# Optimization experiments

Hardware: AMD Instinct MI355X
Metric: run time of the kernel (lower is better)

The kernel has to match this reference:

```python
import jax, jax.numpy as jnp
import numpy as np

H = 32
W = 32
N = H * W            # num_patches = 1024
DIM = 512
HEADS = 8
DH = 64              # dim_head
INNER = HEADS * DH
B = 4
GATE = -2.0          # fixed, requires_grad=False in the torch module
NEG_THRESH = 0.9


def _rel_pos_index_dis():
    # mirrors relative_pos_index_dis(height=32, weight=32)
    coords = np.stack(np.meshgrid(np.arange(H), np.arange(W), indexing='ij'))  # [2,H,W]
    flat = coords.reshape(2, -1)                      # [2, N]
    rel = flat[:, :, None] - flat[:, None, :]         # [2, N, N]
    rel = rel.transpose(1, 2, 0).copy()               # [N, N, 2]
    dis = (rel[..., 0].astype(np.float32) / H) ** 2 + (rel[..., 1].astype(np.float32) / W) ** 2
    rel[..., 0] += H - 1
    rel[..., 1] += W - 1
    rel[..., 0] *= 2 * W - 1
    idx = rel.sum(-1)
    return idx.astype(np.int32), dis.astype(np.float32)


def setup_inputs() -> dict:
    key = jax.random.key(0)
    ks = jax.random.split(key, 6)
    rpi, dis = _rel_pos_index_dis()
    return {
        'x': jax.random.normal(ks[0], (B, N, DIM), dtype=jnp.float32),
        'prob': jax.random.uniform(ks[1], (B, N), dtype=jnp.float32),
        'w_qkv': jax.random.normal(ks[2], (DIM, 3 * INNER), dtype=jnp.float32) * 0.02,
        'rpb_table': jax.random.normal(ks[3], ((2 * H - 1) * (2 * W - 1), HEADS), dtype=jnp.float32) * 0.02,
        'headsita': jnp.arange(1, HEADS + 1, dtype=jnp.float32) * 0.1,
        'w_thresh': jax.random.normal(ks[4], (DH,), dtype=jnp.float32) * 0.02,
        'w_out': jax.random.normal(ks[5], (INNER, DIM), dtype=jnp.float32) * 0.02,
        'b_out': jnp.zeros((DIM,), dtype=jnp.float32),
        'rpi': jnp.asarray(rpi),
        'dis': jnp.asarray(dis),
    }


def reference(x, prob, w_qkv, rpb_table, headsita, w_thresh, w_out, b_out, rpi, dis):
    b, n, _ = x.shape
    h = headsita.shape[0]
    d = w_thresh.shape[0]
    scale = d ** -0.5

    qkv = x @ w_qkv                                            # [b, n, 3*h*d]
    q, k, v = jnp.split(qkv, 3, axis=-1)
    to_heads = lambda t: t.reshape(b, n, h, d).transpose(0, 2, 1, 3)  # [b, h, n, d]
    q, k, v = to_heads(q), to_heads(k), to_heads(v)

    dots0 = jnp.einsum('bhid,bhjd->bhij', q, k) * scale        # [b, h, n, n]

    # RPE: table lookup bias + learned Gaussian distance bias
    rpb = rpb_table[rpi.reshape(-1)].reshape(n, n, h).transpose(2, 0, 1)  # [h, n, n]
    factor = 1.0 / (2.0 * headsita ** 2 + 1e-6)                # [h]
    pos = jnp.exp(-factor[:, None, None] * dis[None, :, :])    # [h, n, n]
    dots = dots0 + rpb[None] + 0.01 * pos[None]

    attn = jax.nn.softmax(dots, axis=-1)                       # [b, h, n, n]
    attn_max = attn.max(axis=-1)                               # [b, h, n]
    attn_min = attn.min(axis=-1)

    # per-query learned threshold, gated by sigmoid(gate)
    t = jax.nn.sigmoid(jnp.einsum('bhnd,d->bhn', q, w_thresh)) * jax.nn.sigmoid(GATE)
    thresh = attn_min + t * (attn_max - attn_min)               # [b, h, n]

    record = (attn - thresh[..., None] > 0).astype(attn.dtype)  # hard 0/1 mask
    # rows (queries) whose prob >= neg_thresh are fully zeroed (as in the torch code)
    record = record * (prob < NEG_THRESH)[:, None, :, None].astype(attn.dtype)

    deno = jnp.sum(attn * record, axis=-1)                      # [b, h, n]
    attn_p = attn * record / (deno[..., None] + 1e-6)

    out = jnp.einsum('bhij,bhjd->bhid', attn_p, v)              # [b, h, n, d]
    out = out.transpose(0, 2, 1, 3).reshape(b, n, h * d)
    out = out @ w_out + b_out                                   # [b, n, dim]
    return out, jax.nn.softmax(dots0, axis=-1)
```

## Files before the change

### kernel.cpp

```cpp
#include <hip/hip_runtime.h>


__device__ __forceinline__ float wsum(float v) {
#pragma unroll
  for (int off = 32; off > 0; off >>= 1) v += __shfl_xor(v, off, 64);
  return v;
}
__device__ __forceinline__ float wmaxr(float v) {
#pragma unroll
  for (int off = 32; off > 0; off >>= 1) v = fmaxf(v, __shfl_xor(v, off, 64));
  return v;
}
__device__ __forceinline__ float wminr(float v) {
#pragma unroll
  for (int off = 32; off > 0; off >>= 1) v = fminf(v, __shfl_xor(v, off, 64));
  return v;
}

__global__ __launch_bounds__(256) void gemm_f32_128(
    const float* __restrict__ A, const float* __restrict__ Bm,
    float* __restrict__ C, int M, int N, int K) {
  __shared__ float As[16][132];
  __shared__ float Bs[16][132];
  const int t = threadIdx.x;
  const int bm = blockIdx.y * 128;
  const int bn = blockIdx.x * 128;
  const int tx = t & 15;
  const int ty = t >> 4;

  float acc[8][8];
#pragma unroll
  for (int i = 0; i < 8; ++i)
#pragma unroll
    for (int j = 0; j < 8; ++j) acc[i][j] = 0.0f;

  const int mr = t >> 1;
  const int kc = (t & 1) * 8;
  const int kr = t >> 4;
  const int nc = (t & 15) * 8;

  for (int k0 = 0; k0 < K; k0 += 16) {
    const float4* asrc = (const float4*)&A[(size_t)(bm + mr) * K + k0 + kc];
    const float4 a0 = asrc[0], a1 = asrc[1];
    const float4* bsrc = (const float4*)&Bm[(size_t)(k0 + kr) * N + bn + nc];
    const float4 b0 = bsrc[0], b1 = bsrc[1];
    __syncthreads();
    As[kc + 0][mr] = a0.x; As[kc + 1][mr] = a0.y;
    As[kc + 2][mr] = a0.z; As[kc + 3][mr] = a0.w;
    As[kc + 4][mr] = a1.x; As[kc + 5][mr] = a1.y;
    As[kc + 6][mr] = a1.z; As[kc + 7][mr] = a1.w;
    *(float4*)&Bs[kr][nc] = b0;
    *(float4*)&Bs[kr][nc + 4] = b1;
    __syncthreads();
#pragma unroll
    for (int kk = 0; kk < 16; ++kk) {
      const float4 aLo = *(const float4*)&As[kk][ty * 4];
      const float4 aHi = *(const float4*)&As[kk][64 + ty * 4];
      const float4 bLo = *(const float4*)&Bs[kk][tx * 4];
      const float4 bHi = *(const float4*)&Bs[kk][64 + tx * 4];
      const float av[8] = {aLo.x, aLo.y, aLo.z, aLo.w, aHi.x, aHi.y, aHi.z, aHi.w};
      const float bv[8] = {bLo.x, bLo.y, bLo.z, bLo.w, bHi.x, bHi.y, bHi.z, bHi.w};
#pragma unroll
      for (int i = 0; i < 8; ++i)
#pragma unroll
        for (int j = 0; j < 8; ++j) acc[i][j] += av[i] * bv[j];
    }
  }

#pragma unroll
  for (int i = 0; i < 8; ++i) {
    const int row = bm + ((i < 4) ? (ty * 4 + i) : (64 + ty * 4 + (i - 4)));
    float4 lo, hi;
    lo.x = acc[i][0]; lo.y = acc[i][1]; lo.z = acc[i][2]; lo.w = acc[i][3];
    hi.x = acc[i][4]; hi.y = acc[i][5]; hi.z = acc[i][6]; hi.w = acc[i][7];
    *(float4*)&C[(size_t)row * N + bn + tx * 4] = lo;
    *(float4*)&C[(size_t)row * N + bn + 64 + tx * 4] = hi;
  }
}

__global__ __launch_bounds__(256, 2) void attn_fused(
    const float* __restrict__ qkv,
    const float* __restrict__ prob,
    const float* __restrict__ rpb,
    const float* __restrict__ headsita,
    const float* __restrict__ w_thresh,
    float* __restrict__ out2,
    float* __restrict__ attnout)
{
  __shared__ float kv_lds[128 * 64];
  __shared__ float q_t[64 * 32];
  __shared__ float multi[4096];

  const int t = threadIdx.x;
  const int w = t >> 6;
  const int l = t & 63;
  const int itile = blockIdx.x;
  const int bh = blockIdx.y;
  const int b = bh >> 3;
  const int h = bh & 7;
  const int i0 = itile * 32;
  const int yi = itile;

#pragma unroll
  for (int c = 0; c < 8; ++c) {
    const int e = c * 256 + t;
    if (e < 2016) multi[e] = rpb[(size_t)(yi * 63 + e) * 8 + h];
  }
#pragma unroll
  for (int c = 0; c < 8; ++c) {
    const int idx = c * 256 + t;
    const int row = idx >> 6, d = idx & 63;
    q_t[d * 32 + row] = qkv[(size_t)(b * 1024 + i0 + row) * 1536 + h * 64 + d];
  }
  __syncthreads();

  const float sita = headsita[h];
  const float factor = 1.0f / (2.0f * sita * sita + 1e-6f);
  const float wt = w_thresh[l];

  float tval[8], probv[8];
#pragma unroll
  for (int r = 0; r < 8; ++r) {
    const int row = w * 8 + r;
    float v = q_t[l * 32 + row] * wt;
    v = wsum(v);
    tval[r] = (1.0f / (1.0f + __expf(-v))) * 0.11920292202211755f;
    probv[r] = prob[b * 1024 + i0 + row];
  }

  float s[8][16];
#pragma unroll
  for (int r = 0; r < 8; ++r)
#pragma unroll
    for (int tt = 0; tt < 16; ++tt) s[r][tt] = 0.0f;

  const size_t kbase = (size_t)b * 1024 * 1536 + 512 + h * 64;
  const int swl = l & 31;
#pragma unroll
  for (int jt = 0; jt < 8; ++jt) {
    __syncthreads();
#pragma unroll
    for (int c = 0; c < 8; ++c) {
      const int f = (c * 256 + t) * 4;
      const int j = f >> 6, d = f & 63;
      const float4 v4 = *(const float4*)&qkv[kbase + (size_t)(jt * 128 + j) * 1536 + d];
      const int sw = j & 31;
      kv_lds[j * 64 + ((d + 0) ^ sw)] = v4.x;
      kv_lds[j * 64 + ((d + 1) ^ sw)] = v4.y;
      kv_lds[j * 64 + ((d + 2) ^ sw)] = v4.z;
      kv_lds[j * 64 + ((d + 3) ^ sw)] = v4.w;
    }
    __syncthreads();
#pragma unroll 8
    for (int d = 0; d < 64; ++d) {
      const float kv0 = kv_lds[l * 64 + (d ^ swl)];
      const float kv1 = kv_lds[(64 + l) * 64 + (d ^ swl)];
      const float4 qA = *(const float4*)&q_t[d * 32 + w * 8];
      const float4 qB = *(const float4*)&q_t[d * 32 + w * 8 + 4];
      const float qa[8] = {qA.x, qA.y, qA.z, qA.w, qB.x, qB.y, qB.z, qB.w};
#pragma unroll
      for (int r = 0; r < 8; ++r) {
        s[r][jt * 2 + 0] += qa[r] * kv0;
        s[r][jt * 2 + 1] += qa[r] * kv1;
      }
    }
  }

  const size_t o2base = ((size_t)(b * 8 + h)) * 1024 * 1024;
#pragma unroll
  for (int r = 0; r < 8; ++r) {
#pragma unroll
    for (int tt = 0; tt < 16; ++tt) s[r][tt] *= 0.125f;
    float m = -1e30f;
#pragma unroll
    for (int tt = 0; tt < 16; ++tt) m = fmaxf(m, s[r][tt]);
    m = wmaxr(m);
    float e[16];
    float sum = 0.0f;
#pragma unroll
    for (int tt = 0; tt < 16; ++tt) { e[tt] = __expf(s[r][tt] - m); sum += e[tt]; }
    sum = wsum(sum);
    const float inv = 1.0f / sum;
    float* orow = out2 + o2base + (size_t)(i0 + w * 8 + r) * 1024;
#pragma unroll
    for (int tt = 0; tt < 16; ++tt)
      __builtin_nontemporal_store(e[tt] * inv, &orow[tt * 64 + l]);
  }

#pragma unroll
  for (int r = 0; r < 8; ++r) {
    const int xi = (w * 8 + r) & 31;
#pragma unroll
    for (int tt = 0; tt < 16; ++tt) {
      const int j = tt * 64 + l;
      const int yj = j >> 5, xj = j & 31;
      const float rpbv = multi[(31 - yj) * 63 + (xi - xj + 31)];
      const float dy = (float)(yi - yj) * 0.03125f;
      const float dx = (float)(xi - xj) * 0.03125f;
      s[r][tt] += rpbv + 0.01f * __expf(-factor * (dy * dy + dx * dx));
    }
  }

#pragma unroll
  for (int r = 0; r < 8; ++r) {
    float m = -1e30f, mn = 1e30f;
#pragma unroll
    for (int tt = 0; tt < 16; ++tt) { m = fmaxf(m, s[r][tt]); mn = fminf(mn, s[r][tt]); }
    m = wmaxr(m); mn = wminr(mn);
    float sum = 0.0f;
#pragma unroll
    for (int tt = 0; tt < 16; ++tt) { const float e = __expf(s[r][tt] - m); s[r][tt] = e; sum += e; }
    sum = wsum(sum);
    const float invd = 1.0f / sum;
    const float amax = invd;
    const float amin = __expf(mn - m) * invd;
    const float th = amin + tval[r] * (amax - amin);
    const float ok = (probv[r] < 0.9f) ? 1.0f : 0.0f;
    float deno = 0.0f;
#pragma unroll
    for (int tt = 0; tt < 16; ++tt) {
      float a = s[r][tt] * invd * ok;
      a = (a > th) ? a : 0.0f;
      s[r][tt] = a;
      deno += a;
    }
    deno = wsum(deno);
    const float invden = 1.0f / (deno + 1e-6f);
#pragma unroll
    for (int tt = 0; tt < 16; ++tt) s[r][tt] *= invden;
  }

  float outv[8];
#pragma unroll
  for (int r = 0; r < 8; ++r) outv[r] = 0.0f;
  const size_t vbase = (size_t)b * 1024 * 1536 + 1024 + h * 64;
#pragma unroll
  for (int jt = 0; jt < 8; ++jt) {
    __syncthreads();
#pragma unroll
    for (int u = 0; u < 2; ++u)
#pragma unroll
      for (int r = 0; r < 8; ++r)
        multi[(w * 128 + u * 64 + l) * 8 + r] = s[r][jt * 2 + u];
#pragma unroll
    for (int c = 0; c < 8; ++c) {
      const int f = (c * 256 + t) * 4;
      const int j = f >> 6, d = f & 63;
      const float4 v4 = *(const float4*)&qkv[vbase + (size_t)(jt * 128 + j) * 1536 + d];
      const int sw = j & 31;
      kv_lds[j * 64 + ((d + 0) ^ sw)] = v4.x;
      kv_lds[j * 64 + ((d + 1) ^ sw)] = v4.y;
      kv_lds[j * 64 + ((d + 2) ^ sw)] = v4.z;
      kv_lds[j * 64 + ((d + 3) ^ sw)] = v4.w;
    }
    __syncthreads();
#pragma unroll 4
    for (int j = 0; j < 128; ++j) {
      const float vv = kv_lds[j * 64 + (l ^ (j & 31))];
      const float4 pA = *(const float4*)&multi[(w * 128 + j) * 8];
      const float4 pB = *(const float4*)&multi[(w * 128 + j) * 8 + 4];
      outv[0] += pA.x * vv; outv[1] += pA.y * vv;
      outv[2] += pA.z * vv; outv[3] += pA.w * vv;
      outv[4] += pB.x * vv; outv[5] += pB.y * vv;
      outv[6] += pB.z * vv; outv[7] += pB.w * vv;
    }
  }
#pragma unroll
  for (int r = 0; r < 8; ++r)
    attnout[(size_t)(b * 1024 + i0 + w * 8 + r) * 512 + h * 64 + l] = outv[r];
}

__global__ __launch_bounds__(256) void gemm_f32_64_bias(
    const float* __restrict__ A, const float* __restrict__ Bm,
    const float* __restrict__ bias, float* __restrict__ C,
    int M, int N, int K) {
  __shared__ float As[16][68];
  __shared__ float Bs[16][68];
  const int t = threadIdx.x;
  const int bm = blockIdx.y * 64;
  const int bn = blockIdx.x * 64;
  const int tx = t & 15;
  const int ty = t >> 4;

  float acc[4][4];
#pragma unroll
  for (int i = 0; i < 4; ++i)
#pragma unroll
    for (int j = 0; j < 4; ++j) acc[i][j] = 0.0f;

  const int amr = t >> 2;
  const int akc = (t & 3) * 4;
  const int bkr = t >> 4;
  const int bnc = (t & 15) * 4;

  for (int k0 = 0; k0 < K; k0 += 16) {
    const float4 a0 = *(const float4*)&A[(size_t)(bm + amr) * K + k0 + akc];
    const float4 b0 = *(const float4*)&Bm[(size_t)(k0 + bkr) * N + bn + bnc];
    __syncthreads();
    As[akc + 0][amr] = a0.x; As[akc + 1][amr] = a0.y;
    As[akc + 2][amr] = a0.z; As[akc + 3][amr] = a0.w;
    *(float4*)&Bs[bkr][bnc] = b0;
    __syncthreads();
#pragma unroll
    for (int kk = 0; kk < 16; ++kk) {
      const float4 av = *(const float4*)&As[kk][ty * 4];
      const float4 bv = *(const float4*)&Bs[kk][tx * 4];
      const float aa[4] = {av.x, av.y, av.z, av.w};
      const float bb[4] = {bv.x, bv.y, bv.z, bv.w};
#pragma unroll
      for (int i = 0; i < 4; ++i)
#pragma unroll
        for (int j = 0; j < 4; ++j) acc[i][j] += aa[i] * bb[j];
    }
  }

  const float4 bi = *(const float4*)&bias[bn + tx * 4];
#pragma unroll
  for (int i = 0; i < 4; ++i) {
    float4 o;
    o.x = acc[i][0] + bi.x; o.y = acc[i][1] + bi.y;
    o.z = acc[i][2] + bi.z; o.w = acc[i][3] + bi.w;
    *(float4*)&C[(size_t)(bm + ty * 4 + i) * N + bn + tx * 4] = o;
  }
}

extern "C" void kernel_launch(void* const* d_in, const int* in_sizes, int n_in,
                              void* d_out, int out_size, void* d_ws, size_t ws_size,
                              hipStream_t stream) {
  const float* x        = (const float*)d_in[0];
  const float* prob     = (const float*)d_in[1];
  const float* w_qkv    = (const float*)d_in[2];
  const float* rpb      = (const float*)d_in[3];
  const float* headsita = (const float*)d_in[4];
  const float* w_thresh = (const float*)d_in[5];
  const float* w_out    = (const float*)d_in[6];
  const float* b_out    = (const float*)d_in[7];

  float* out  = (float*)d_out;
  float* out2 = out + (size_t)4 * 1024 * 512;

  float* qkv     = (float*)d_ws;
  float* attnout = qkv + (size_t)4 * 1024 * 1536;

  gemm_f32_128<<<dim3(1536 / 128, 4096 / 128), 256, 0, stream>>>(
      x, w_qkv, qkv, 4096, 1536, 512);

  attn_fused<<<dim3(32, 32), 256, 0, stream>>>(
      qkv, prob, rpb, headsita, w_thresh, out2, attnout);

  gemm_f32_64_bias<<<dim3(512 / 64, 4096 / 64), 256, 0, stream>>>(
      attnout, w_out, b_out, out, 4096, 512, 512);
}
```

Before: 514.5 us.

## Precompute bias table, vectorize LDS layouts, and simplify threshold math in attention

Adds a small kernel that folds the relative-position bias and the Gaussian distance term into one per-head table, so the attention kernel no longer evaluates an exp per score. The K and V tiles are stored in LDS with float4 XOR swizzles (V transposed) so inner loops use vector LDS reads. Probabilities are staged per row instead of interleaved. The threshold and masking are done on unnormalized exponentials, with the prob mask folded into the threshold value. Launch bounds are raised on all kernels to target higher occupancy, which risks register spills.

New measurement: 590.9 us. 14.8% more time.

```diff
diff --git a/kernel.cpp b/kernel.cpp
--- a/kernel.cpp
+++ b/kernel.cpp
@@ -17,7 +17,22 @@
   return v;
 }
 
-__global__ __launch_bounds__(256) void gemm_f32_128(
+__global__ void build_btab(const float* __restrict__ rpb,
+                           const float* __restrict__ headsita,
+                           float* __restrict__ btab) {
+  const int h = blockIdx.y;
+  const int flat = blockIdx.x * 256 + threadIdx.x;
+  if (flat >= 3969) return;
+  const float sita = headsita[h];
+  const float factor = 1.0f / (2.0f * sita * sita + 1e-6f);
+  const int dy = flat / 63 - 31;
+  const int dx = flat % 63 - 31;
+  const float fy = (float)dy * 0.03125f, fx = (float)dx * 0.03125f;
+  btab[h * 3969 + flat] =
+      rpb[(size_t)flat * 8 + h] + 0.01f * __expf(-factor * (fy * fy + fx * fx));
+}
+
+__global__ __launch_bounds__(256, 4) void gemm_f32_128(
     const float* __restrict__ A, const float* __restrict__ Bm,
     float* __restrict__ C, int M, int N, int K) {
   __shared__ float As[16][132];
@@ -78,54 +93,48 @@
   }
 }
 
-__global__ __launch_bounds__(256, 2) void attn_fused(
+__global__ __launch_bounds__(256, 3) void attn_fused(
     const float* __restrict__ qkv,
     const float* __restrict__ prob,
-    const float* __restrict__ rpb,
-    const float* __restrict__ headsita,
+    const float* __restrict__ btab,
     const float* __restrict__ w_thresh,
     float* __restrict__ out2,
     float* __restrict__ attnout)
 {
   __shared__ float kv_lds[128 * 64];
-  __shared__ float q_t[64 * 32];
-  __shared__ float multi[4096];
+  __shared__ float q_t[64 * 36];
+  __shared__ float multi[2080];
 
   const int t = threadIdx.x;
-  const int w = t >> 6;
-  const int l = t & 63;
+  const int w = t >> 6, l = t & 63;
   const int itile = blockIdx.x;
   const int bh = blockIdx.y;
-  const int b = bh >> 3;
-  const int h = bh & 7;
+  const int b = bh >> 3, h = bh & 7;
   const int i0 = itile * 32;
   const int yi = itile;
 
+  const float* bsl = btab + h * 3969 + yi * 63;
 #pragma unroll
   for (int c = 0; c < 8; ++c) {
     const int e = c * 256 + t;
-    if (e < 2016) multi[e] = rpb[(size_t)(yi * 63 + e) * 8 + h];
+    if (e < 2016) multi[e] = bsl[e];
   }
 #pragma unroll
   for (int c = 0; c < 8; ++c) {
     const int idx = c * 256 + t;
     const int row = idx >> 6, d = idx & 63;
-    q_t[d * 32 + row] = qkv[(size_t)(b * 1024 + i0 + row) * 1536 + h * 64 + d];
+    q_t[d * 36 + row] = qkv[(size_t)(b * 1024 + i0 + row) * 1536 + h * 64 + d];
   }
   __syncthreads();
 
-  const float sita = headsita[h];
-  const float factor = 1.0f / (2.0f * sita * sita + 1e-6f);
   const float wt = w_thresh[l];
-
-  float tval[8], probv[8];
 #pragma unroll
   for (int r = 0; r < 8; ++r) {
     const int row = w * 8 + r;
-    float v = q_t[l * 32 + row] * wt;
-    v = wsum(v);
-    tval[r] = (1.0f / (1.0f + __expf(-v))) * 0.11920292202211755f;
-    probv[r] = prob[b * 1024 + i0 + row];
+    const float v = wsum(q_t[l * 36 + row] * wt);
+    float tv = (1.0f / (1.0f + __expf(-v))) * 0.11920292202211755f;
+    tv += (prob[b * 1024 + i0 + row] >= 0.9f) ? 2.0f : 0.0f;
+    multi[2048 + w * 8 + r] = tv;
   }
 
   float s[8][16];
@@ -135,38 +144,39 @@
     for (int tt = 0; tt < 16; ++tt) s[r][tt] = 0.0f;
 
   const size_t kbase = (size_t)b * 1024 * 1536 + 512 + h * 64;
-  const int swl = l & 31;
 #pragma unroll
   for (int jt = 0; jt < 8; ++jt) {
     __syncthreads();
 #pragma unroll
     for (int c = 0; c < 8; ++c) {
       const int f = (c * 256 + t) * 4;
-      const int j = f >> 6, d = f & 63;
-      const float4 v4 = *(const float4*)&qkv[kbase + (size_t)(jt * 128 + j) * 1536 + d];
-      const int sw = j & 31;
-      kv_lds[j * 64 + ((d + 0) ^ sw)] = v4.x;
-      kv_lds[j * 64 + ((d + 1) ^ sw)] = v4.y;
-      kv_lds[j * 64 + ((d + 2) ^ sw)] = v4.z;
-      kv_lds[j * 64 + ((d + 3) ^ sw)] = v4.w;
-    }
-    __syncthreads();
-#pragma unroll 8
-    for (int d = 0; d < 64; ++d) {
-      const float kv0 = kv_lds[l * 64 + (d ^ swl)];
-      const float kv1 = kv_lds[(64 + l) * 64 + (d ^ swl)];
-      const float4 qA = *(const float4*)&q_t[d * 32 + w * 8];
-      const float4 qB = *(const float4*)&q_t[d * 32 + w * 8 + 4];
-      const float qa[8] = {qA.x, qA.y, qA.z, qA.w, qB.x, qB.y, qB.z, qB.w};
-#pragma unroll
-      for (int r = 0; r < 8; ++r) {
-        s[r][jt * 2 + 0] += qa[r] * kv0;
-        s[r][jt * 2 + 1] += qa[r] * kv1;
+      const int j = f >> 6, dd = f & 63;
+      const float4 v4 = *(const float4*)&qkv[kbase + (size_t)(jt * 128 + j) * 1536 + dd];
+      *(float4*)&kv_lds[j * 64 + 4 * ((dd >> 2) ^ (j & 15))] = v4;
+    }
+    __syncthreads();
+#pragma unroll 4
+    for (int d0 = 0; d0 < 64; d0 += 4) {
+      const int g = 4 * ((d0 >> 2) ^ (l & 15));
+      const float4 ka = *(const float4*)&kv_lds[l * 64 + g];
+      const float4 kb = *(const float4*)&kv_lds[(64 + l) * 64 + g];
+      const float ka4[4] = {ka.x, ka.y, ka.z, ka.w};
+      const float kb4[4] = {kb.x, kb.y, kb.z, kb.w};
+#pragma unroll
+      for (int i = 0; i < 4; ++i) {
+        const float4 qA = *(const float4*)&q_t[(d0 + i) * 36 + w * 8];
+        const float4 qB = *(const float4*)&q_t[(d0 + i) * 36 + w * 8 + 4];
+        const float qa[8] = {qA.x, qA.y, qA.z, qA.w, qB.x, qB.y, qB.z, qB.w};
+#pragma unroll
+        for (int r = 0; r < 8; ++r) {
+          s[r][jt * 2 + 0] += qa[r] * ka4[i];
+          s[r][jt * 2 + 1] += qa[r] * kb4[i];
+        }
       }
     }
   }
 
-  const size_t o2base = ((size_t)(b * 8 + h)) * 1024 * 1024;
+  const size_t o2base = ((size_t)(b * 8 + h)) << 20;
 #pragma unroll
   for (int r = 0; r < 8; ++r) {
 #pragma unroll
@@ -175,16 +185,15 @@
 #pragma unroll
     for (int tt = 0; tt < 16; ++tt) m = fmaxf(m, s[r][tt]);
     m = wmaxr(m);
-    float e[16];
     float sum = 0.0f;
 #pragma unroll
-    for (int tt = 0; tt < 16; ++tt) { e[tt] = __expf(s[r][tt] - m); sum += e[tt]; }
+    for (int tt = 0; tt < 16; ++tt) sum += __expf(s[r][tt] - m);
     sum = wsum(sum);
     const float inv = 1.0f / sum;
     float* orow = out2 + o2base + (size_t)(i0 + w * 8 + r) * 1024;
 #pragma unroll
     for (int tt = 0; tt < 16; ++tt)
-      __builtin_nontemporal_store(e[tt] * inv, &orow[tt * 64 + l]);
+      __builtin_nontemporal_store(__expf(s[r][tt] - m) * inv, &orow[tt * 64 + l]);
   }
 
 #pragma unroll
@@ -194,10 +203,7 @@
     for (int tt = 0; tt < 16; ++tt) {
       const int j = tt * 64 + l;
       const int yj = j >> 5, xj = j & 31;
-      const float rpbv = multi[(31 - yj) * 63 + (xi - xj + 31)];
-      const float dy = (float)(yi - yj) * 0.03125f;
-      const float dx = (float)(xi - xj) * 0.03125f;
-      s[r][tt] += rpbv + 0.01f * __expf(-factor * (dy * dy + dx * dx));
+      s[r][tt] += multi[(31 - yj) * 63 + (xi - xj + 31)];
     }
   }
 
@@ -211,21 +217,18 @@
 #pragma unroll
     for (int tt = 0; tt < 16; ++tt) { const float e = __expf(s[r][tt] - m); s[r][tt] = e; sum += e; }
     sum = wsum(sum);
-    const float invd = 1.0f / sum;
-    const float amax = invd;
-    const float amin = __expf(mn - m) * invd;
-    const float th = amin + tval[r] * (amax - amin);
-    const float ok = (probv[r] < 0.9f) ? 1.0f : 0.0f;
+    const float emin = __expf(mn - m);
+    const float tv = multi[2048 + w * 8 + r];
+    const float th_e = emin + tv * (1.0f - emin);
     float deno = 0.0f;
 #pragma unroll
     for (int tt = 0; tt < 16; ++tt) {
-      float a = s[r][tt] * invd * ok;
-      a = (a > th) ? a : 0.0f;
+      const float a = (s[r][tt] > th_e) ? s[r][tt] : 0.0f;
       s[r][tt] = a;
       deno += a;
     }
     deno = wsum(deno);
-    const float invden = 1.0f / (deno + 1e-6f);
+    const float invden = 1.0f / (deno + 1e-6f * sum);
 #pragma unroll
     for (int tt = 0; tt < 16; ++tt) s[r][tt] *= invden;
   }
@@ -238,31 +241,31 @@
   for (int jt = 0; jt < 8; ++jt) {
     __syncthreads();
 #pragma unroll
-    for (int u = 0; u < 2; ++u)
-#pragma unroll
-      for (int r = 0; r < 8; ++r)
-        multi[(w * 128 + u * 64 + l) * 8 + r] = s[r][jt * 2 + u];
-#pragma unroll
     for (int c = 0; c < 8; ++c) {
       const int f = (c * 256 + t) * 4;
-      const int j = f >> 6, d = f & 63;
-      const float4 v4 = *(const float4*)&qkv[vbase + (size_t)(jt * 128 + j) * 1536 + d];
-      const int sw = j & 31;
-      kv_lds[j * 64 + ((d + 0) ^ sw)] = v4.x;
-      kv_lds[j * 64 + ((d + 1) ^ sw)] = v4.y;
-      kv_lds[j * 64 + ((d + 2) ^ sw)] = v4.z;
-      kv_lds[j * 64 + ((d + 3) ^ sw)] = v4.w;
-    }
-    __syncthreads();
+      const int j = f >> 6, dd = f & 63;
+      const float4 v4 = *(const float4*)&qkv[vbase + (size_t)(jt * 128 + j) * 1536 + dd];
+      const float vv4[4] = {v4.x, v4.y, v4.z, v4.w};
+#pragma unroll
+      for (int i = 0; i < 4; ++i)
+        kv_lds[(dd + i) * 128 + 4 * ((j >> 2) ^ ((dd + i) & 15)) + (j & 3)] = vv4[i];
+    }
+    __syncthreads();
+#pragma unroll
+    for (int h2 = 0; h2 < 2; ++h2) {
+#pragma unroll
+      for (int r = 0; r < 8; ++r) multi[w * 512 + r * 64 + l] = s[r][jt * 2 + h2];
 #pragma unroll 4
-    for (int j = 0; j < 128; ++j) {
-      const float vv = kv_lds[j * 64 + (l ^ (j & 31))];
-      const float4 pA = *(const float4*)&multi[(w * 128 + j) * 8];
-      const float4 pB = *(const float4*)&multi[(w * 128 + j) * 8 + 4];
-      outv[0] += pA.x * vv; outv[1] += pA.y * vv;
-      outv[2] += pA.z * vv; outv[3] += pA.w * vv;
-      outv[4] += pB.x * vv; outv[5] += pB.y * vv;
-      outv[6] += pB.z * vv; outv[7] += pB.w * vv;
+      for (int j0 = 0; j0 < 64; j0 += 4) {
+        const int jc = h2 * 64 + j0;
+        const float4 vv = *(const float4*)&kv_lds[l * 128 + 4 * ((jc >> 2) ^ (l & 15))];
+        const float vvv[4] = {vv.x, vv.y, vv.z, vv.w};
+#pragma unroll
+        for (int r = 0; r < 8; ++r) {
+          const float4 p4 = *(const float4*)&multi[w * 512 + r * 64 + j0];
+          outv[r] += p4.x * vvv[0] + p4.y * vvv[1] + p4.z * vvv[2] + p4.w * vvv[3];
+        }
+      }
     }
   }
 #pragma unroll
@@ -270,7 +273,7 @@
     attnout[(size_t)(b * 1024 + i0 + w * 8 + r) * 512 + h * 64 + l] = outv[r];
 }
 
-__global__ __launch_bounds__(256) void gemm_f32_64_bias(
+__global__ __launch_bounds__(256, 4) void gemm_f32_64_bias(
     const float* __restrict__ A, const float* __restrict__ Bm,
     const float* __restrict__ bias, float* __restrict__ C,
     int M, int N, int K) {
@@ -341,12 +344,15 @@
 
   float* qkv     = (float*)d_ws;
   float* attnout = qkv + (size_t)4 * 1024 * 1536;
+  float* btab    = attnout + (size_t)4 * 1024 * 512;
+
+  build_btab<<<dim3(16, 8), 256, 0, stream>>>(rpb, headsita, btab);
 
   gemm_f32_128<<<dim3(1536 / 128, 4096 / 128), 256, 0, stream>>>(
       x, w_qkv, qkv, 4096, 1536, 512);
 
   attn_fused<<<dim3(32, 32), 256, 0, stream>>>(
-      qkv, prob, rpb, headsita, w_thresh, out2, attnout);
+      qkv, prob, btab, w_thresh, out2, attnout);
 
   gemm_f32_64_bias<<<dim3(512 / 64, 4096 / 64), 256, 0, stream>>>(
       attnout, w_out, b_out, out, 4096, 512, 512);
```
